# Kernel optimization log

Measured on AMD Instinct MI355X. Metric: run time of the kernel, lower is better.

Reference implementation:

```python
import jax, jax.numpy as jnp
import numpy as np

D_MODEL = 1024
N_HEADS = 16
D_KV = D_MODEL // N_HEADS
MAX_SEQ = 2048
THETA = 10000.0
BATCH = 2
SEQ = 2048


def setup_inputs() -> dict:
    key = jax.random.key(0)
    ks = jax.random.split(key, 5)
    std = np.sqrt(2.0 / (D_MODEL + D_MODEL))
    x = jax.random.normal(ks[0], (BATCH, SEQ, D_MODEL), dtype=jnp.float32)
    wq = jax.random.normal(ks[1], (D_MODEL, D_MODEL), dtype=jnp.float32) * std
    wk = jax.random.normal(ks[2], (D_MODEL, D_MODEL), dtype=jnp.float32) * std
    wv = jax.random.normal(ks[3], (D_MODEL, D_MODEL), dtype=jnp.float32) * std
    wo = jax.random.normal(ks[4], (D_MODEL, D_MODEL), dtype=jnp.float32) * std
    token_positions = jnp.arange(SEQ, dtype=jnp.int32)
    return {"x": x, "wq": wq, "wk": wk, "wv": wv, "wo": wo,
            "token_positions": token_positions}


def _rope_tables():
    freq_range = jnp.arange(D_KV // 2, dtype=jnp.float32)
    freq = 1.0 / (THETA ** (2.0 * freq_range / D_KV))
    pos = jnp.arange(MAX_SEQ, dtype=jnp.float32)
    angs = pos[:, None] * freq[None, :]  # [max_seq, d_kv/2]
    return jnp.cos(angs), jnp.sin(angs)


def _apply_rope(xh, token_positions, cos_t, sin_t):
    # xh: [b, h, s, d_kv]
    cos_f = jnp.repeat(cos_t[token_positions], 2, axis=-1)  # [s, d_kv]
    sin_f = jnp.repeat(sin_t[token_positions], 2, axis=-1)
    pairs = xh.reshape(*xh.shape[:-1], D_KV // 2, 2)
    even, odd = pairs[..., 0], pairs[..., 1]
    rot = jnp.stack([-odd, even], axis=-1).reshape(xh.shape)
    return xh * cos_f + rot * sin_f


def reference(x, wq, wk, wv, wo, token_positions):
    b, s, _ = x.shape
    def heads(y):
        return y.reshape(b, s, N_HEADS, D_KV).transpose(0, 2, 1, 3)  # [b,h,s,d]
    q = heads(jnp.einsum('bsi,oi->bso', x, wq))
    k = heads(jnp.einsum('bsi,oi->bso', x, wk))
    v = heads(jnp.einsum('bsi,oi->bso', x, wv))
    cos_t, sin_t = _rope_tables()
    q = _apply_rope(q, token_positions, cos_t, sin_t)
    k = _apply_rope(k, token_positions, cos_t, sin_t)
    scale = 1.0 / jnp.sqrt(jnp.asarray(D_KV, x.dtype))
    scores = jnp.einsum('bhqd,bhkd->bhqk', q, k) * scale
    causal = jnp.tril(jnp.ones((s, s), dtype=bool))
    scores = jnp.where(causal, scores, -jnp.inf)
    probs = jax.nn.softmax(scores, axis=-1)
    attn = jnp.einsum('bhqk,bhkd->bhqd', probs, v)
    attn = attn.transpose(0, 2, 1, 3).reshape(b, s, D_MODEL)
    return jnp.einsum('bsi,oi->bso', attn, wo)
```

## Files before the change

kernel.cpp:

```cpp
#include <hip/hip_runtime.h>
#include <hip/hip_bf16.h>
#include <math.h>

#define SEQ 2048
#define DM 1024
#define NH 16
#define DKV 64
#define MTOT 4096
#define PST2 72

typedef __attribute__((ext_vector_type(8))) short bf16x8;
typedef __attribute__((ext_vector_type(4))) short s16x4;
typedef __attribute__((ext_vector_type(4))) float f32x4;
typedef unsigned short ushort_t;

__device__ __forceinline__ short f2bf(float f) {
    union { float f; unsigned u; } v; v.f = f;
    unsigned r = v.u + 0x7fffu + ((v.u >> 16) & 1u);
    return (short)(r >> 16);
}

__device__ __forceinline__ bf16x8 cvt8(f32x4 a, f32x4 b) {
    union { __hip_bfloat162 h[4]; bf16x8 v; } u;
    u.h[0] = __float22bfloat162_rn(float2{a[0], a[1]});
    u.h[1] = __float22bfloat162_rn(float2{a[2], a[3]});
    u.h[2] = __float22bfloat162_rn(float2{b[0], b[1]});
    u.h[3] = __float22bfloat162_rn(float2{b[2], b[3]});
    return u.v;
}

__device__ __forceinline__ s16x4 cvt4(float a, float b, float c, float d) {
    union { __hip_bfloat162 h[2]; s16x4 v; } u;
    u.h[0] = __float22bfloat162_rn(float2{a, b});
    u.h[1] = __float22bfloat162_rn(float2{c, d});
    return u.v;
}

__device__ __forceinline__ void gload_lds16(const void* g, void* l) {
    __builtin_amdgcn_global_load_lds(
        (const __attribute__((address_space(1))) unsigned int*)g,
        (__attribute__((address_space(3))) unsigned int*)l, 16, 0, 0);
}

__global__ void prep_kernel(const float* __restrict__ x,
                            const float* __restrict__ wq, const float* __restrict__ wk,
                            const float* __restrict__ wv,
                            ushort_t* __restrict__ Wqkv, ushort_t* __restrict__ xb,
                            float* __restrict__ cos_t, float* __restrict__ sin_t) {
    const int b = blockIdx.x;
    if (b < 256) {
        int tid = b * 256 + threadIdx.x;
        int i = tid & 31, pos = tid >> 5;
        float freq = expf(-9.210340372f * (float)(2 * i) / 64.0f);
        float ang = (float)pos * freq;
        cos_t[tid] = cosf(ang);
        sin_t[tid] = sinf(ang);
    } else if (b < 1792) {
        int tid = (b - 256) * 256 + threadIdx.x;
        int z = tid >> 17;
        int off = (tid & 131071) * 8;
        const float* src = (z == 0) ? wq : (z == 1) ? wk : wv;
        f32x4 a = ((const f32x4*)(src + off))[0];
        f32x4 c = ((const f32x4*)(src + off))[1];
        *(bf16x8*)&Wqkv[(size_t)z * 1048576 + off] = cvt8(a, c);
    } else {
        int tid = (b - 1792) * 256 + threadIdx.x;
        int off = tid * 8;
        f32x4 a = ((const f32x4*)(x + off))[0];
        f32x4 c = ((const f32x4*)(x + off))[1];
        *(bf16x8*)&xb[off] = cvt8(a, c);
    }
}

__global__ void cvt_f2b_kernel(const float* __restrict__ src, ushort_t* __restrict__ dst) {
    int tid = blockIdx.x * blockDim.x + threadIdx.x;
    int off = tid * 8;
    f32x4 a = ((const f32x4*)(src + off))[0];
    f32x4 b = ((const f32x4*)(src + off))[1];
    *(bf16x8*)&dst[off] = cvt8(a, b);
}

__global__ __launch_bounds__(256) void proj_qkv_kernel(
    const ushort_t* __restrict__ xb, const ushort_t* __restrict__ Wqkv,
    const float* __restrict__ cos_t, const float* __restrict__ sin_t,
    const int* __restrict__ tokpos,
    ushort_t* __restrict__ Qg, ushort_t* __restrict__ Kg, ushort_t* __restrict__ Vt)
{
    __shared__ __align__(16) short lA[3][128 * 32];
    __shared__ __align__(16) short lB[3][64 * 32];

    const int t = threadIdx.x;
    const int lane = t & 63;
    const int wid = t >> 6;
    const int quad = lane >> 4, l16 = lane & 15;
    const int mh = wid >> 1, nh = wid & 1;
    const int Mb = blockIdx.y * 128;
    const int NbG = blockIdx.x * 64;
    const int z = NbG >> 10;
    const int Nb = NbG & 1023;

    f32x4 acc[4][2] = {};

    auto stage = [&](int buf, int k0) {
        #pragma unroll
        for (int i = 0; i < 2; ++i) {
            int rbase = wid * 32 + i * 16;
            int row = rbase + (lane >> 2);
            int gch = (lane & 3) ^ ((lane >> 3) & 3);
            gload_lds16(xb + (size_t)(Mb + row) * DM + k0 + gch * 8, &lA[buf][rbase * 32]);
        }
        {
            int rbase = wid * 16;
            int row = rbase + (lane >> 2);
            int gch = (lane & 3) ^ ((lane >> 3) & 3);
            gload_lds16(Wqkv + (size_t)(NbG + row) * DM + k0 + gch * 8, &lB[buf][rbase * 32]);
        }
    };

    stage(0, 0);
    stage(1, 32);

    for (int kt = 0; kt < 32; ++kt) {
        const int cur = kt % 3;
        if (kt == 31) asm volatile("s_waitcnt vmcnt(0)" ::: "memory");
        else          asm volatile("s_waitcnt vmcnt(3)" ::: "memory");
        __builtin_amdgcn_s_barrier();
        if (kt < 30) stage((kt + 2) % 3, kt * 32 + 64);

        bf16x8 a[4], b[2];
        #pragma unroll
        for (int mt = 0; mt < 4; ++mt) {
            int row = mh * 64 + mt * 16 + l16;
            int slot = quad ^ ((l16 >> 1) & 3);
            a[mt] = *(const bf16x8*)&lA[cur][row * 32 + slot * 8];
        }
        #pragma unroll
        for (int nt = 0; nt < 2; ++nt) {
            int row = nh * 32 + nt * 16 + l16;
            int slot = quad ^ ((l16 >> 1) & 3);
            b[nt] = *(const bf16x8*)&lB[cur][row * 32 + slot * 8];
        }
        __builtin_amdgcn_s_setprio(1);
        #pragma unroll
        for (int mt = 0; mt < 4; ++mt)
            #pragma unroll
            for (int nt = 0; nt < 2; ++nt)
                acc[mt][nt] = __builtin_amdgcn_mfma_f32_16x16x32_bf16(a[mt], b[nt], acc[mt][nt], 0, 0, 0);
        __builtin_amdgcn_s_setprio(0);
    }

    const int bb = Mb >> 11;
    if (z == 2) {
        #pragma unroll
        for (int mt = 0; mt < 4; ++mt) {
            const int s0 = (Mb + mh * 64 + mt * 16 + quad * 4) & (SEQ - 1);
            #pragma unroll
            for (int nt = 0; nt < 2; ++nt) {
                int col = Nb + nh * 32 + nt * 16 + l16;
                int h = col >> 6, d = col & 63;
                s16x4 pk;
                #pragma unroll
                for (int r = 0; r < 4; ++r) pk[r] = f2bf(acc[mt][nt][r]);
                *(s16x4*)&Vt[((size_t)(bb * NH + h) * DKV + d) * SEQ + s0] = pk;
            }
        }
    } else {
        ushort_t* dst = (z == 0) ? Qg : Kg;
        const float qscale = (z == 0) ? 0.125f : 1.0f;
        #pragma unroll
        for (int mt = 0; mt < 4; ++mt) {
            #pragma unroll
            for (int nt = 0; nt < 2; ++nt) {
                #pragma unroll
                for (int r = 0; r < 4; ++r) {
                    int row = Mb + mh * 64 + mt * 16 + quad * 4 + r;
                    int s = row & (SEQ - 1);
                    int col = Nb + nh * 32 + nt * 16 + l16;
                    int h = col >> 6, d = col & 63;
                    float val = acc[mt][nt][r];
                    float part = __shfl_xor(val, 1, 64);
                    int pos = tokpos[s];
                    int i = d >> 1;
                    float c = cos_t[pos * 32 + i];
                    float sn = sin_t[pos * 32 + i];
                    val = (d & 1) ? (val * c + part * sn) : (val * c - part * sn);
                    val *= qscale;
                    dst[((size_t)(bb * NH + h) * SEQ + s) * DKV + d] = (ushort_t)f2bf(val);
                }
            }
        }
    }
}

__global__ __launch_bounds__(256, 2) void attn_kernel(
    const ushort_t* __restrict__ Q, const ushort_t* __restrict__ K,
    const ushort_t* __restrict__ Vt, ushort_t* __restrict__ O)
{
    __shared__ __align__(16) short lK[2][64 * 64];
    __shared__ __align__(16) short lV[2][64 * 64];
    __shared__ __align__(16) short lP[4][16 * PST2];

    const int t = threadIdx.x;
    const int lane = t & 63;
    const int wid = t >> 6;
    const int quad = lane >> 4, l16 = lane & 15;
    const int bh = blockIdx.y;
    const int bb = bh >> 4, h = bh & 15;

    const ushort_t* Qb = Q + (size_t)bh * SEQ * DKV;
    const ushort_t* Kb = K + (size_t)bh * SEQ * DKV;
    const ushort_t* Vtb = Vt + (size_t)bh * DKV * SEQ;
    short* myP = lP[wid];

    auto stage = [&](int kb, int buf) {
        #pragma unroll
        for (int j = 0; j < 2; ++j) {
            int rbase = wid * 16 + j * 8;
            int row = rbase + (lane >> 3);
            int gch = (lane & 7) ^ (row & 7);
            gload_lds16(Kb + (size_t)(kb + row) * DKV + gch * 8, &lK[buf][rbase * 64]);
        }
        #pragma unroll
        for (int j = 0; j < 2; ++j) {
            int rbase = wid * 16 + j * 8;
            int row = rbase + (lane >> 3);
            int gch = (lane & 7) ^ (row & 7);
            gload_lds16(Vtb + (size_t)row * SEQ + kb + gch * 8, &lV[buf][rbase * 64]);
        }
    };

    #pragma unroll 1
    for (int ph = 0; ph < 2; ++ph) {
        const int qt = ph ? (31 - (int)blockIdx.x) : (int)blockIdx.x;
        const int q0w = qt * 64 + wid * 16;
        const int nkt = qt + 1;

        bf16x8 bq[2];
        #pragma unroll
        for (int hq = 0; hq < 2; ++hq)
            bq[hq] = *(const bf16x8*)(Qb + (size_t)(q0w + l16) * DKV + hq * 32 + quad * 8);

        f32x4 acc[4] = {};
        float ps = 0.f;

        if (ph) __syncthreads();
        stage(0, 0);

        for (int kt = 0; kt < nkt; ++kt) {
            const int kbase = kt * 64;
            __syncthreads();
            if (kt + 1 < nkt) stage(kbase + 64, (kt + 1) & 1);

            const short* bK = lK[kt & 1];
            const short* bV = lV[kt & 1];

            bf16x8 ak[4][2];
            #pragma unroll
            for (int mt = 0; mt < 4; ++mt)
                #pragma unroll
                for (int hh = 0; hh < 2; ++hh) {
                    int row = mt * 16 + l16;
                    int slot = (hh * 4 + quad) ^ (row & 7);
                    ak[mt][hh] = *(const bf16x8*)&bK[row * 64 + slot * 8];
                }

            f32x4 st[4];
            __builtin_amdgcn_s_setprio(1);
            #pragma unroll
            for (int mt = 0; mt < 4; ++mt) {
                f32x4 zz = {};
                zz = __builtin_amdgcn_mfma_f32_16x16x32_bf16(ak[mt][0], bq[0], zz, 0, 0, 0);
                zz = __builtin_amdgcn_mfma_f32_16x16x32_bf16(ak[mt][1], bq[1], zz, 0, 0, 0);
                st[mt] = zz;
            }
            __builtin_amdgcn_s_setprio(0);

            if (kbase + 63 > q0w) {
                #pragma unroll
                for (int mt = 0; mt < 4; ++mt) {
                    float pv[4];
                    #pragma unroll
                    for (int r = 0; r < 4; ++r) {
                        int k_abs = kbase + mt * 16 + quad * 4 + r;
                        int q_abs = q0w + l16;
                        pv[r] = (k_abs > q_abs) ? 0.f : __expf(st[mt][r]);
                        ps += pv[r];
                    }
                    *(s16x4*)&myP[l16 * PST2 + mt * 16 + quad * 4] = cvt4(pv[0], pv[1], pv[2], pv[3]);
                }
            } else {
                #pragma unroll
                for (int mt = 0; mt < 4; ++mt) {
                    float pv[4];
                    #pragma unroll
                    for (int r = 0; r < 4; ++r) {
                        pv[r] = __expf(st[mt][r]);
                        ps += pv[r];
                    }
                    *(s16x4*)&myP[l16 * PST2 + mt * 16 + quad * 4] = cvt4(pv[0], pv[1], pv[2], pv[3]);
                }
            }

            bf16x8 ap[2];
            ap[0] = *(const bf16x8*)&myP[l16 * PST2 + quad * 8];
            ap[1] = *(const bf16x8*)&myP[l16 * PST2 + 32 + quad * 8];

            __builtin_amdgcn_s_setprio(1);
            #pragma unroll
            for (int d = 0; d < 4; ++d) {
                int row = d * 16 + l16;
                int slot0 = quad ^ (row & 7);
                int slot1 = (4 + quad) ^ (row & 7);
                bf16x8 bv0 = *(const bf16x8*)&bV[row * 64 + slot0 * 8];
                bf16x8 bv1 = *(const bf16x8*)&bV[row * 64 + slot1 * 8];
                acc[d] = __builtin_amdgcn_mfma_f32_16x16x32_bf16(ap[0], bv0, acc[d], 0, 0, 0);
                acc[d] = __builtin_amdgcn_mfma_f32_16x16x32_bf16(ap[1], bv1, acc[d], 0, 0, 0);
            }
            __builtin_amdgcn_s_setprio(0);
        }

        ps += __shfl_xor(ps, 16, 64);
        ps += __shfl_xor(ps, 32, 64);
        float* lLw = (float*)myP;
        if (quad == 0) lLw[l16] = ps;
        f32x4 lv = *(const f32x4*)&lLw[quad * 4];
        f32x4 inv;
        #pragma unroll
        for (int r = 0; r < 4; ++r) inv[r] = 1.0f / lv[r];
        #pragma unroll
        for (int d = 0; d < 4; ++d)
            #pragma unroll
            for (int r = 0; r < 4; ++r) {
                int qrow = q0w + quad * 4 + r;
                int dd = d * 16 + l16;
                O[(size_t)(bb * SEQ + qrow) * DM + h * DKV + dd] = (ushort_t)f2bf(acc[d][r] * inv[r]);
            }
    }
}

__global__ __launch_bounds__(256) void oproj_kernel(
    const ushort_t* __restrict__ A, const ushort_t* __restrict__ B, float* __restrict__ out)
{
    __shared__ __align__(16) short lA[3][128 * 32];
    __shared__ __align__(16) short lB[3][64 * 32];

    const int t = threadIdx.x;
    const int lane = t & 63;
    const int wid = t >> 6;
    const int quad = lane >> 4, l16 = lane & 15;
    const int mh = wid >> 1, nh = wid & 1;
    const int Mb = blockIdx.y * 128;
    const int Nb = blockIdx.x * 64;

    f32x4 acc[4][2] = {};

    auto stage = [&](int buf, int k0) {
        #pragma unroll
        for (int i = 0; i < 2; ++i) {
            int rbase = wid * 32 + i * 16;
            int row = rbase + (lane >> 2);
            int gch = (lane & 3) ^ ((lane >> 3) & 3);
            gload_lds16(A + (size_t)(Mb + row) * DM + k0 + gch * 8, &lA[buf][rbase * 32]);
        }
        {
            int rbase = wid * 16;
            int row = rbase + (lane >> 2);
            int gch = (lane & 3) ^ ((lane >> 3) & 3);
            gload_lds16(B + (size_t)(Nb + row) * DM + k0 + gch * 8, &lB[buf][rbase * 32]);
        }
    };

    stage(0, 0);
    stage(1, 32);

    for (int kt = 0; kt < 32; ++kt) {
        const int cur = kt % 3;
        if (kt == 31) asm volatile("s_waitcnt vmcnt(0)" ::: "memory");
        else          asm volatile("s_waitcnt vmcnt(3)" ::: "memory");
        __builtin_amdgcn_s_barrier();
        if (kt < 30) stage((kt + 2) % 3, kt * 32 + 64);

        bf16x8 a[4], b[2];
        #pragma unroll
        for (int mt = 0; mt < 4; ++mt) {
            int row = mh * 64 + mt * 16 + l16;
            int slot = quad ^ ((l16 >> 1) & 3);
            a[mt] = *(const bf16x8*)&lA[cur][row * 32 + slot * 8];
        }
        #pragma unroll
        for (int nt = 0; nt < 2; ++nt) {
            int row = nh * 32 + nt * 16 + l16;
            int slot = quad ^ ((l16 >> 1) & 3);
            b[nt] = *(const bf16x8*)&lB[cur][row * 32 + slot * 8];
        }
        __builtin_amdgcn_s_setprio(1);
        #pragma unroll
        for (int mt = 0; mt < 4; ++mt)
            #pragma unroll
            for (int nt = 0; nt < 2; ++nt)
                acc[mt][nt] = __builtin_amdgcn_mfma_f32_16x16x32_bf16(a[mt], b[nt], acc[mt][nt], 0, 0, 0);
        __builtin_amdgcn_s_setprio(0);
    }

    #pragma unroll
    for (int mt = 0; mt < 4; ++mt)
        #pragma unroll
        for (int nt = 0; nt < 2; ++nt)
            #pragma unroll
            for (int r = 0; r < 4; ++r) {
                int row = Mb + mh * 64 + mt * 16 + quad * 4 + r;
                int col = Nb + nh * 32 + nt * 16 + l16;
                out[(size_t)row * DM + col] = acc[mt][nt][r];
            }
}

extern "C" void kernel_launch(void* const* d_in, const int* in_sizes, int n_in,
                              void* d_out, int out_size, void* d_ws, size_t ws_size,
                              hipStream_t stream) {
    const float* x  = (const float*)d_in[0];
    const float* wq = (const float*)d_in[1];
    const float* wk = (const float*)d_in[2];
    const float* wv = (const float*)d_in[3];
    const float* wo = (const float*)d_in[4];
    const int* tokpos = (const int*)d_in[5];
    float* out = (float*)d_out;

    char* ws = (char*)d_ws;
    float* cos_t    = (float*)ws;
    float* sin_t    = (float*)(ws + 256 * 1024);
    ushort_t* Wqkv  = (ushort_t*)(ws + 512 * 1024);
    ushort_t* AO    = (ushort_t*)ws;
    ushort_t* Qg    = (ushort_t*)(ws + (size_t)8  * 1024 * 1024);
    ushort_t* Kg    = (ushort_t*)(ws + (size_t)16 * 1024 * 1024);
    ushort_t* Vt    = (ushort_t*)(ws + (size_t)24 * 1024 * 1024);
    ushort_t* Wob   = Qg;
    ushort_t* xb    = (ushort_t*)d_out;

    prep_kernel<<<3840, 256, 0, stream>>>(x, wq, wk, wv, Wqkv, xb, cos_t, sin_t);
    proj_qkv_kernel<<<dim3(3 * DM / 64, MTOT / 128), 256, 0, stream>>>(
        xb, Wqkv, cos_t, sin_t, tokpos, Qg, Kg, Vt);
    attn_kernel<<<dim3(SEQ / 128, 32), 256, 0, stream>>>(Qg, Kg, Vt, AO);
    cvt_f2b_kernel<<<512, 256, 0, stream>>>(wo, Wob);
    oproj_kernel<<<dim3(DM / 64, MTOT / 128), 256, 0, stream>>>(AO, Wob, out);
}
```

Before: 204.0 us.

## Use barrier-free single-wave GEMM blocks with double buffering in projections

The QKV and output projection GEMMs move from 4-wave 256-thread blocks with a triple-buffered LDS pipeline and per-iteration barriers to single-wave 64-thread blocks with double buffering and no barrier. QKV tiles become 64x64 per wave and output projection tiles become 64x32, and the grids grow to match. The aim is to drop barrier synchronisation and raise block count and occupancy. In exchange each tile reuses fewer loaded operands, so global and LDS traffic per FLOP goes up, and prefetch depth falls from two stages to one.

```diff
diff --git a/kernel.cpp b/kernel.cpp
--- a/kernel.cpp
+++ b/kernel.cpp
@@ -80,37 +80,35 @@
     *(bf16x8*)&dst[off] = cvt8(a, b);
 }
 
-__global__ __launch_bounds__(256) void proj_qkv_kernel(
+__global__ __launch_bounds__(64) void proj_qkv_kernel(
     const ushort_t* __restrict__ xb, const ushort_t* __restrict__ Wqkv,
     const float* __restrict__ cos_t, const float* __restrict__ sin_t,
     const int* __restrict__ tokpos,
     ushort_t* __restrict__ Qg, ushort_t* __restrict__ Kg, ushort_t* __restrict__ Vt)
 {
-    __shared__ __align__(16) short lA[3][128 * 32];
-    __shared__ __align__(16) short lB[3][64 * 32];
-
-    const int t = threadIdx.x;
-    const int lane = t & 63;
-    const int wid = t >> 6;
+    __shared__ __align__(16) short lA[2][64 * 32];
+    __shared__ __align__(16) short lB[2][64 * 32];
+
+    const int lane = threadIdx.x;
     const int quad = lane >> 4, l16 = lane & 15;
-    const int mh = wid >> 1, nh = wid & 1;
-    const int Mb = blockIdx.y * 128;
+    const int Mb = blockIdx.y * 64;
     const int NbG = blockIdx.x * 64;
     const int z = NbG >> 10;
     const int Nb = NbG & 1023;
 
-    f32x4 acc[4][2] = {};
+    f32x4 acc[4][4] = {};
 
     auto stage = [&](int buf, int k0) {
         #pragma unroll
-        for (int i = 0; i < 2; ++i) {
-            int rbase = wid * 32 + i * 16;
+        for (int i = 0; i < 4; ++i) {
+            int rbase = i * 16;
             int row = rbase + (lane >> 2);
             int gch = (lane & 3) ^ ((lane >> 3) & 3);
             gload_lds16(xb + (size_t)(Mb + row) * DM + k0 + gch * 8, &lA[buf][rbase * 32]);
         }
-        {
-            int rbase = wid * 16;
+        #pragma unroll
+        for (int i = 0; i < 4; ++i) {
+            int rbase = i * 16;
             int row = rbase + (lane >> 2);
             int gch = (lane & 3) ^ ((lane >> 3) & 3);
             gload_lds16(Wqkv + (size_t)(NbG + row) * DM + k0 + gch * 8, &lB[buf][rbase * 32]);
@@ -118,25 +116,23 @@
     };
 
     stage(0, 0);
-    stage(1, 32);
 
     for (int kt = 0; kt < 32; ++kt) {
-        const int cur = kt % 3;
+        const int cur = kt & 1;
+        if (kt < 31) stage(cur ^ 1, kt * 32 + 32);
         if (kt == 31) asm volatile("s_waitcnt vmcnt(0)" ::: "memory");
-        else          asm volatile("s_waitcnt vmcnt(3)" ::: "memory");
-        __builtin_amdgcn_s_barrier();
-        if (kt < 30) stage((kt + 2) % 3, kt * 32 + 64);
-
-        bf16x8 a[4], b[2];
+        else          asm volatile("s_waitcnt vmcnt(8)" ::: "memory");
+
+        bf16x8 a[4], b[4];
         #pragma unroll
         for (int mt = 0; mt < 4; ++mt) {
-            int row = mh * 64 + mt * 16 + l16;
+            int row = mt * 16 + l16;
             int slot = quad ^ ((l16 >> 1) & 3);
             a[mt] = *(const bf16x8*)&lA[cur][row * 32 + slot * 8];
         }
         #pragma unroll
-        for (int nt = 0; nt < 2; ++nt) {
-            int row = nh * 32 + nt * 16 + l16;
+        for (int nt = 0; nt < 4; ++nt) {
+            int row = nt * 16 + l16;
             int slot = quad ^ ((l16 >> 1) & 3);
             b[nt] = *(const bf16x8*)&lB[cur][row * 32 + slot * 8];
         }
@@ -144,7 +140,7 @@
         #pragma unroll
         for (int mt = 0; mt < 4; ++mt)
             #pragma unroll
-            for (int nt = 0; nt < 2; ++nt)
+            for (int nt = 0; nt < 4; ++nt)
                 acc[mt][nt] = __builtin_amdgcn_mfma_f32_16x16x32_bf16(a[mt], b[nt], acc[mt][nt], 0, 0, 0);
         __builtin_amdgcn_s_setprio(0);
     }
@@ -153,10 +149,10 @@
     if (z == 2) {
         #pragma unroll
         for (int mt = 0; mt < 4; ++mt) {
-            const int s0 = (Mb + mh * 64 + mt * 16 + quad * 4) & (SEQ - 1);
-            #pragma unroll
-            for (int nt = 0; nt < 2; ++nt) {
-                int col = Nb + nh * 32 + nt * 16 + l16;
+            const int s0 = (Mb + mt * 16 + quad * 4) & (SEQ - 1);
+            #pragma unroll
+            for (int nt = 0; nt < 4; ++nt) {
+                int col = Nb + nt * 16 + l16;
                 int h = col >> 6, d = col & 63;
                 s16x4 pk;
                 #pragma unroll
@@ -170,12 +166,12 @@
         #pragma unroll
         for (int mt = 0; mt < 4; ++mt) {
             #pragma unroll
-            for (int nt = 0; nt < 2; ++nt) {
+            for (int nt = 0; nt < 4; ++nt) {
                 #pragma unroll
                 for (int r = 0; r < 4; ++r) {
-                    int row = Mb + mh * 64 + mt * 16 + quad * 4 + r;
+                    int row = Mb + mt * 16 + quad * 4 + r;
                     int s = row & (SEQ - 1);
-                    int col = Nb + nh * 32 + nt * 16 + l16;
+                    int col = Nb + nt * 16 + l16;
                     int h = col >> 6, d = col & 63;
                     float val = acc[mt][nt][r];
                     float part = __shfl_xor(val, 1, 64);
@@ -338,32 +334,30 @@
     }
 }
 
-__global__ __launch_bounds__(256) void oproj_kernel(
+__global__ __launch_bounds__(64) void oproj_kernel(
     const ushort_t* __restrict__ A, const ushort_t* __restrict__ B, float* __restrict__ out)
 {
-    __shared__ __align__(16) short lA[3][128 * 32];
-    __shared__ __align__(16) short lB[3][64 * 32];
-
-    const int t = threadIdx.x;
-    const int lane = t & 63;
-    const int wid = t >> 6;
+    __shared__ __align__(16) short lA[2][64 * 32];
+    __shared__ __align__(16) short lB[2][32 * 32];
+
+    const int lane = threadIdx.x;
     const int quad = lane >> 4, l16 = lane & 15;
-    const int mh = wid >> 1, nh = wid & 1;
-    const int Mb = blockIdx.y * 128;
-    const int Nb = blockIdx.x * 64;
+    const int Mb = blockIdx.y * 64;
+    const int Nb = blockIdx.x * 32;
 
     f32x4 acc[4][2] = {};
 
     auto stage = [&](int buf, int k0) {
         #pragma unroll
-        for (int i = 0; i < 2; ++i) {
-            int rbase = wid * 32 + i * 16;
+        for (int i = 0; i < 4; ++i) {
+            int rbase = i * 16;
             int row = rbase + (lane >> 2);
             int gch = (lane & 3) ^ ((lane >> 3) & 3);
             gload_lds16(A + (size_t)(Mb + row) * DM + k0 + gch * 8, &lA[buf][rbase * 32]);
         }
-        {
-            int rbase = wid * 16;
+        #pragma unroll
+        for (int i = 0; i < 2; ++i) {
+            int rbase = i * 16;
             int row = rbase + (lane >> 2);
             int gch = (lane & 3) ^ ((lane >> 3) & 3);
             gload_lds16(B + (size_t)(Nb + row) * DM + k0 + gch * 8, &lB[buf][rbase * 32]);
@@ -371,25 +365,23 @@
     };
 
     stage(0, 0);
-    stage(1, 32);
 
     for (int kt = 0; kt < 32; ++kt) {
-        const int cur = kt % 3;
+        const int cur = kt & 1;
+        if (kt < 31) stage(cur ^ 1, kt * 32 + 32);
         if (kt == 31) asm volatile("s_waitcnt vmcnt(0)" ::: "memory");
-        else          asm volatile("s_waitcnt vmcnt(3)" ::: "memory");
-        __builtin_amdgcn_s_barrier();
-        if (kt < 30) stage((kt + 2) % 3, kt * 32 + 64);
+        else          asm volatile("s_waitcnt vmcnt(6)" ::: "memory");
 
         bf16x8 a[4], b[2];
         #pragma unroll
         for (int mt = 0; mt < 4; ++mt) {
-            int row = mh * 64 + mt * 16 + l16;
+            int row = mt * 16 + l16;
             int slot = quad ^ ((l16 >> 1) & 3);
             a[mt] = *(const bf16x8*)&lA[cur][row * 32 + slot * 8];
         }
         #pragma unroll
         for (int nt = 0; nt < 2; ++nt) {
-            int row = nh * 32 + nt * 16 + l16;
+            int row = nt * 16 + l16;
             int slot = quad ^ ((l16 >> 1) & 3);
             b[nt] = *(const bf16x8*)&lB[cur][row * 32 + slot * 8];
         }
@@ -408,8 +400,8 @@
         for (int nt = 0; nt < 2; ++nt)
             #pragma unroll
             for (int r = 0; r < 4; ++r) {
-                int row = Mb + mh * 64 + mt * 16 + quad * 4 + r;
-                int col = Nb + nh * 32 + nt * 16 + l16;
+                int row = Mb + mt * 16 + quad * 4 + r;
+                int col = Nb + nt * 16 + l16;
                 out[(size_t)row * DM + col] = acc[mt][nt][r];
             }
 }
@@ -437,9 +429,9 @@
     ushort_t* xb    = (ushort_t*)d_out;
 
     prep_kernel<<<3840, 256, 0, stream>>>(x, wq, wk, wv, Wqkv, xb, cos_t, sin_t);
-    proj_qkv_kernel<<<dim3(3 * DM / 64, MTOT / 128), 256, 0, stream>>>(
+    proj_qkv_kernel<<<dim3(3 * DM / 64, MTOT / 64), 64, 0, stream>>>(
         xb, Wqkv, cos_t, sin_t, tokpos, Qg, Kg, Vt);
     attn_kernel<<<dim3(SEQ / 128, 32), 256, 0, stream>>>(Qg, Kg, Vt, AO);
     cvt_f2b_kernel<<<512, 256, 0, stream>>>(wo, Wob);
-    oproj_kernel<<<dim3(DM / 64, MTOT / 128), 256, 0, stream>>>(AO, Wob, out);
-}
+    oproj_kernel<<<dim3(DM / 32, MTOT / 64), 64, 0, stream>>>(AO, Wob, out);
+}
```

Measured after the change: 214.2 us. +5.0%, slower.
